# Kernel optimization log

Measured on AMD Instinct MI355X. Metric: run time of the kernel, lower is better.

## Reference

```python
import jax, jax.numpy as jnp
import numpy as np

N = 50000   # nodes
E = 800000  # edges
D = 128     # node feature dim
H = 128     # hidden channels
G = 500     # graphs
EPS = 1e-5


def setup_inputs() -> dict:
    key = jax.random.key(0)
    ks = jax.random.split(key, 12)
    s = 0.05
    inp = {
        'x': jax.random.normal(ks[0], (N, D), jnp.float32),
        'edge_index': jax.random.randint(ks[1], (2, E), 0, N, jnp.int64),
        'batch': jnp.sort(jax.random.randint(ks[2], (N,), 0, G, jnp.int64)),
        'W1': jax.random.normal(ks[3], (D, H), jnp.float32) * s,
        'b1': jnp.zeros((H,), jnp.float32),
        'g1': jnp.ones((H,), jnp.float32),
        'be1': jnp.zeros((H,), jnp.float32),
        'W2': jax.random.normal(ks[4], (H, H), jnp.float32) * s,
        'b2': jnp.zeros((H,), jnp.float32),
        'g2': jnp.ones((H,), jnp.float32),
        'be2': jnp.zeros((H,), jnp.float32),
        'W3': jax.random.normal(ks[5], (H, H), jnp.float32) * s,
        'b3': jnp.zeros((H,), jnp.float32),
        'g3': jnp.ones((H,), jnp.float32),
        'be3': jnp.zeros((H,), jnp.float32),
        'fcW1': jax.random.normal(ks[6], (H, H // 2), jnp.float32) * s,
        'fcb1': jnp.zeros((H // 2,), jnp.float32),
        'fcg1': jnp.ones((H // 2,), jnp.float32),
        'fcbe1': jnp.zeros((H // 2,), jnp.float32),
        'fcW2': jax.random.normal(ks[7], (H // 2, 1), jnp.float32) * s,
        'fcb2': jnp.zeros((1,), jnp.float32),
    }
    return inp


def _bn(h, g, b):
    # training-mode BatchNorm1d: batch stats, biased variance
    m = h.mean(0)
    v = jnp.mean((h - m) ** 2, 0)
    return g * (h - m) * jax.lax.rsqrt(v + EPS) + b


def reference(x, edge_index, batch, W1, b1, g1, be1, W2, b2, g2, be2,
              W3, b3, g3, be3, fcW1, fcb1, fcg1, fcbe1, fcW2, fcb2):
    # GCN normalization with self-loops: D^{-1/2}(A+I)D^{-1/2}
    loop = jnp.arange(N, dtype=edge_index.dtype)
    src = jnp.concatenate([edge_index[0], loop])
    dst = jnp.concatenate([edge_index[1], loop])
    deg = jax.ops.segment_sum(jnp.ones_like(dst, dtype=x.dtype), dst, N)
    dis = jax.lax.rsqrt(jnp.maximum(deg, 1.0))  # deg>=1 due to self loops
    norm = dis[src] * dis[dst]  # [E+N]

    def conv_bn_relu(h, W, b, g, be):
        h = h @ W                                   # [N,H]
        msg = h[src] * norm[:, None]                # gather + scale
        agg = jax.ops.segment_sum(msg, dst, N) + b  # scatter-add
        return jax.nn.relu(_bn(agg, g, be))

    h = conv_bn_relu(x, W1, b1, g1, be1)
    h = conv_bn_relu(h, W2, b2, g2, be2)
    h = conv_bn_relu(h, W3, b3, g3, be3)

    # global_mean_pool per graph
    cnt = jax.ops.segment_sum(jnp.ones((N,), h.dtype), batch, G)
    pooled = jax.ops.segment_sum(h, batch, G) / jnp.maximum(cnt, 1.0)[:, None]

    z = pooled @ fcW1 + fcb1
    z = jax.nn.relu(_bn(z, fcg1, fcbe1))
    return z @ fcW2 + fcb2  # [G,1]
```

## Files before the change

### kernel.cpp

```cpp
#include <hip/hip_runtime.h>

#define EPS 1e-5f
constexpr int HD = 128;
constexpr int FCD = 64;

typedef __attribute__((ext_vector_type(8))) short short8;
typedef __attribute__((ext_vector_type(4))) float floatx4;

__device__ inline ushort f2bf(float f){
  union{float f; unsigned u;} v; v.f = f;
  unsigned r = v.u + 0x7FFFu + ((v.u >> 16) & 1u);
  return (ushort)(r >> 16);
}
__device__ inline float bflo(unsigned u){ union{unsigned i; float f;} v; v.i = u << 16;        return v.f; }
__device__ inline float bfhi(unsigned u){ union{unsigned i; float f;} v; v.i = u & 0xFFFF0000u; return v.f; }
__device__ inline float bf2f(ushort u){ union{unsigned i; float f;} v; v.i = ((unsigned)u) << 16; return v.f; }


__global__ __launch_bounds__(256) void k_hist(const int* __restrict__ dst,
                                              int* __restrict__ bucketHist, int E){
  __shared__ int h[256];
  int t = threadIdx.x;
  h[t] = 0;
  __syncthreads();
  int base = blockIdx.x*4096;
  #pragma unroll
  for (int k = 0; k < 16; ++k){
    int e = base + k*256 + t;
    if (e < E) atomicAdd(&h[dst[e] >> 8], 1);
  }
  __syncthreads();
  if (h[t]) atomicAdd(&bucketHist[t], h[t]);
}

__global__ __launch_bounds__(256) void k_bscan(const int* __restrict__ bucketHist,
                                               int* __restrict__ bucketBase,
                                               int* __restrict__ bucketCursor){
  __shared__ int wt[4];
  int t = threadIdx.x, lane = t & 63, w = t >> 6;
  int v = bucketHist[t];
  int incl = v;
  #pragma unroll
  for (int o = 1; o < 64; o <<= 1){
    int x = __shfl_up(incl, o, 64);
    if (lane >= o) incl += x;
  }
  if (lane == 63) wt[w] = incl;
  __syncthreads();
  int woff = 0;
  for (int i = 0; i < w; ++i) woff += wt[i];
  int ex = woff + incl - v;
  bucketBase[t] = ex;
  bucketCursor[t] = ex;
}

__global__ __launch_bounds__(256) void k_bucket(const int* __restrict__ src,
                                                const int* __restrict__ dst,
                                                int* __restrict__ bucketCursor,
                                                int2* __restrict__ tmp, int E){
  __shared__ int h[256], ls[256], cur[256], gb[256];
  __shared__ int wt[4];
  __shared__ int2 staged[4096];
  __shared__ unsigned char bos[4096];
  int t = threadIdx.x, lane = t & 63, w = t >> 6;
  int base = blockIdx.x*4096;
  int2 ed[16]; int bk[16];
  h[t] = 0;
  __syncthreads();
  #pragma unroll
  for (int k = 0; k < 16; ++k){
    int e = base + k*256 + t;
    if (e < E){
      int s = src[e], d = dst[e];
      ed[k] = make_int2(s, d);
      bk[k] = d >> 8;
      atomicAdd(&h[bk[k]], 1);
    } else bk[k] = -1;
  }
  __syncthreads();
  int v = h[t];
  int incl = v;
  #pragma unroll
  for (int o = 1; o < 64; o <<= 1){
    int x = __shfl_up(incl, o, 64);
    if (lane >= o) incl += x;
  }
  if (lane == 63) wt[w] = incl;
  __syncthreads();
  int woff = 0;
  for (int i = 0; i < w; ++i) woff += wt[i];
  ls[t] = woff + incl - v;
  cur[t] = ls[t];
  if (v > 0) gb[t] = atomicAdd(&bucketCursor[t], v);
  __syncthreads();
  #pragma unroll
  for (int k = 0; k < 16; ++k){
    if (bk[k] >= 0){
      int lp = atomicAdd(&cur[bk[k]], 1);
      staged[lp] = ed[k];
      bos[lp] = (unsigned char)bk[k];
    }
  }
  __syncthreads();
  int nvalid = min(4096, E - base);
  #pragma unroll
  for (int k = 0; k < 16; ++k){
    int i = k*256 + t;
    if (i < nvalid){
      int b = bos[i];
      tmp[gb[b] + (i - ls[b])] = staged[i];
    }
  }
}

__global__ __launch_bounds__(256) void k_csr(const int2* __restrict__ tmp,
                                             const int* __restrict__ bucketHist,
                                             const int* __restrict__ bucketBase,
                                             int* __restrict__ rowptr,
                                             float* __restrict__ dis,
                                             int* __restrict__ csrc, int N){
  __shared__ int h[256], ls[256], cur[256];
  __shared__ int wt[4];
  __shared__ int stagedSrc[6144];
  int b = blockIdx.x, t = threadIdx.x, lane = t & 63, w = t >> 6;
  int ebase = bucketBase[b];
  int cnt = bucketHist[b];
  int node0 = b << 8;
  h[t] = 0;
  __syncthreads();
  for (int i = t; i < cnt; i += 256){
    int2 e = tmp[ebase + i];
    atomicAdd(&h[e.y - node0], 1);
  }
  __syncthreads();
  int v = h[t];
  int incl = v;
  #pragma unroll
  for (int o = 1; o < 64; o <<= 1){
    int x = __shfl_up(incl, o, 64);
    if (lane >= o) incl += x;
  }
  if (lane == 63) wt[w] = incl;
  __syncthreads();
  int woff = 0;
  for (int i = 0; i < w; ++i) woff += wt[i];
  int ex = woff + incl - v;
  ls[t] = ex; cur[t] = ex;
  int d = node0 + t;
  if (d < N){
    rowptr[d+1] = ebase + ex + v;
    dis[d] = rsqrtf((float)v + 1.0f);
  }
  if (b == 0 && t == 0) rowptr[0] = 0;
  __syncthreads();
  for (int i = t; i < cnt; i += 256){
    int2 e = tmp[ebase + i];
    int lp = atomicAdd(&cur[e.y - node0], 1);
    stagedSrc[lp] = e.x;
  }
  __syncthreads();
  for (int i = t; i < cnt; i += 256)
    csrc[ebase + i] = stagedSrc[i];
}

__global__ void k_prepW(const float* __restrict__ W1, const float* __restrict__ W2,
                        const float* __restrict__ W3, ushort* __restrict__ Wf){
  const float* Ws[3] = {W1, W2, W3};
  int l = blockIdx.y;
  int idx = blockIdx.x*256 + threadIdx.x;
  int k = idx >> 7, n = idx & 127;
  float w = Ws[l][idx];
  int kb = k >> 5, q = (k >> 3) & 3, j = k & 7;
  int nt = n >> 4, col = n & 15;
  Wf[(size_t)l*16384 + (((size_t)(kb*8 + nt)*64 + q*16 + col)*8 + j)] = f2bf(w);
}

template<int MODE>
__global__ __launch_bounds__(256) void k_gemm(const void* __restrict__ Av,
                                              const ushort* __restrict__ Wf,
                                              const float* __restrict__ sums,
                                              const float* __restrict__ g,
                                              const float* __restrict__ be,
                                              const float* __restrict__ dis,
                                              ushort* __restrict__ O, int n, float invN){
  __shared__ float aL[HD], bL[HD];
  int tid = threadIdx.x;
  if (MODE){
    if (tid < HD){
      float m = sums[tid]*invN;
      float var = fmaxf(sums[HD+tid]*invN - m*m, 0.f);
      float Ac = g[tid]*rsqrtf(var + EPS);
      aL[tid] = Ac; bL[tid] = be[tid] - m*Ac;
    }
    __syncthreads();
  }
  int lane = tid & 63, wave = tid >> 6;
  int quad = lane >> 4, r16 = lane & 15;
  int row = blockIdx.x*64 + wave*16 + r16;
  int rowc = min(row, n-1);
  floatx4 acc[8] = {};
  #pragma unroll
  for (int kb = 0; kb < 4; ++kb){
    int k0 = kb*32 + quad*8;
    short8 af;
    if (MODE){
      const ushort* Arow = (const ushort*)Av + (size_t)rowc*HD;
      short8 raw = *(const short8*)(Arow + k0);
      #pragma unroll
      for (int jj = 0; jj < 8; ++jj){
        float f = bf2f((ushort)raw[jj]);
        f = fmaxf(f*aL[k0+jj] + bL[k0+jj], 0.f);
        af[jj] = (short)f2bf(f);
      }
    } else {
      const float* Arow = (const float*)Av + (size_t)rowc*HD;
      float4 x0 = *(const float4*)(Arow + k0);
      float4 x1 = *(const float4*)(Arow + k0 + 4);
      af[0] = (short)f2bf(x0.x); af[1] = (short)f2bf(x0.y);
      af[2] = (short)f2bf(x0.z); af[3] = (short)f2bf(x0.w);
      af[4] = (short)f2bf(x1.x); af[5] = (short)f2bf(x1.y);
      af[6] = (short)f2bf(x1.z); af[7] = (short)f2bf(x1.w);
    }
    const ushort* wp = Wf + ((size_t)(kb*8)*64 + lane)*8;
    #pragma unroll
    for (int nt = 0; nt < 8; ++nt){
      short8 bf = *(const short8*)(wp + (size_t)nt*64*8);
      acc[nt] = __builtin_amdgcn_mfma_f32_16x16x32_bf16(af, bf, acc[nt], 0, 0, 0);
    }
  }
  int rbase = blockIdx.x*64 + wave*16 + quad*4;
  float ds[4];
  #pragma unroll
  for (int r = 0; r < 4; ++r) ds[r] = dis[min(rbase + r, n-1)];
  #pragma unroll
  for (int nt = 0; nt < 8; ++nt){
    #pragma unroll
    for (int r = 0; r < 4; ++r){
      int rr = rbase + r;
      if (rr < n) O[(size_t)rr*HD + nt*16 + r16] = f2bf(acc[nt][r]*ds[r]);
    }
  }
}

__global__ __launch_bounds__(256) void k_gather(const ushort* __restrict__ hw,
                                                const int* __restrict__ rowptr,
                                                const int* __restrict__ csrc,
                                                const float* __restrict__ dis,
                                                ushort* __restrict__ agg,
                                                float* __restrict__ scratch,
                                                float* __restrict__ sums, int N){
  __shared__ float2 sm[4][HD];
  if (blockIdx.x == 0) sums[threadIdx.x] = 0.f;
  int grp = threadIdx.x >> 4, j = threadIdx.x & 15;
  int wave = threadIdx.x >> 6, lane = threadIdx.x & 63;
  int i = blockIdx.x*16 + grp;
  bool valid = (i < N);
  int ic = valid ? i : N-1;
  uint4 q = ((const uint4*)(hw + (size_t)ic*HD))[j];
  float a[8];
  a[0] = bflo(q.x); a[1] = bfhi(q.x);
  a[2] = bflo(q.y); a[3] = bfhi(q.y);
  a[4] = bflo(q.z); a[5] = bfhi(q.z);
  a[6] = bflo(q.w); a[7] = bfhi(q.w);
  int e = rowptr[ic], e1 = rowptr[ic+1];
  #define ADD8(Q) \
    a[0] += bflo(Q.x); a[1] += bfhi(Q.x); \
    a[2] += bflo(Q.y); a[3] += bfhi(Q.y); \
    a[4] += bflo(Q.z); a[5] += bfhi(Q.z); \
    a[6] += bflo(Q.w); a[7] += bfhi(Q.w);
  while (e < e1 && (e & 3)){
    uint4 qq = ((const uint4*)(hw + (size_t)csrc[e]*HD))[j];
    ADD8(qq);
    e++;
  }
  int4 c0, c1;
  if (e + 8 <= e1){
    c0 = *(const int4*)&csrc[e];
    c1 = *(const int4*)&csrc[e+4];
  }
  while (e + 8 <= e1){
    int en = e + 8;
    int4 n0, n1;
    if (en + 8 <= e1){
      n0 = *(const int4*)&csrc[en];
      n1 = *(const int4*)&csrc[en+4];
    }
    uint4 q0 = ((const uint4*)(hw + (size_t)c0.x*HD))[j];
    uint4 q1 = ((const uint4*)(hw + (size_t)c0.y*HD))[j];
    uint4 q2 = ((const uint4*)(hw + (size_t)c0.z*HD))[j];
    uint4 q3 = ((const uint4*)(hw + (size_t)c0.w*HD))[j];
    uint4 q4 = ((const uint4*)(hw + (size_t)c1.x*HD))[j];
    uint4 q5 = ((const uint4*)(hw + (size_t)c1.y*HD))[j];
    uint4 q6 = ((const uint4*)(hw + (size_t)c1.z*HD))[j];
    uint4 q7 = ((const uint4*)(hw + (size_t)c1.w*HD))[j];
    ADD8(q0); ADD8(q1); ADD8(q2); ADD8(q3);
    ADD8(q4); ADD8(q5); ADD8(q6); ADD8(q7);
    c0 = n0; c1 = n1; e = en;
  }
  if (e + 4 <= e1){
    int4 tt = *(const int4*)&csrc[e];
    uint4 q0 = ((const uint4*)(hw + (size_t)tt.x*HD))[j];
    uint4 q1 = ((const uint4*)(hw + (size_t)tt.y*HD))[j];
    uint4 q2 = ((const uint4*)(hw + (size_t)tt.z*HD))[j];
    uint4 q3 = ((const uint4*)(hw + (size_t)tt.w*HD))[j];
    ADD8(q0); ADD8(q1); ADD8(q2); ADD8(q3);
    e += 4;
  }
  for (; e < e1; ++e){
    uint4 qq = ((const uint4*)(hw + (size_t)csrc[e]*HD))[j];
    ADD8(qq);
  }
  #undef ADD8
  float sc = dis[ic];
  #pragma unroll
  for (int k = 0; k < 8; ++k) a[k] *= sc;
  if (valid){
    uint4 o;
    o.x = (unsigned)f2bf(a[0]) | ((unsigned)f2bf(a[1]) << 16);
    o.y = (unsigned)f2bf(a[2]) | ((unsigned)f2bf(a[3]) << 16);
    o.z = (unsigned)f2bf(a[4]) | ((unsigned)f2bf(a[5]) << 16);
    o.w = (unsigned)f2bf(a[6]) | ((unsigned)f2bf(a[7]) << 16);
    ((uint4*)(agg + (size_t)i*HD))[j] = o;
  }
  float z = valid ? 1.f : 0.f;
  #pragma unroll
  for (int k = 0; k < 8; ++k){
    float s = a[k]*z, qq = a[k]*a[k]*z;
    s  += __shfl_xor(s, 16);  s  += __shfl_xor(s, 32);
    qq += __shfl_xor(qq, 16); qq += __shfl_xor(qq, 32);
    if (lane < 16) sm[wave][lane*8 + k] = make_float2(s, qq);
  }
  __syncthreads();
  int t = threadIdx.x;
  if (t < HD){
    float2 r0 = sm[0][t], r1 = sm[1][t], r2 = sm[2][t], r3 = sm[3][t];
    scratch[(size_t)blockIdx.x*256 + t]      = r0.x + r1.x + r2.x + r3.x;
    scratch[(size_t)blockIdx.x*256 + HD + t] = r0.y + r1.y + r2.y + r3.y;
  }
}

__global__ __launch_bounds__(256) void k_reduce(const float* __restrict__ scratch,
                                                float* __restrict__ sums, int R){
  int t = threadIdx.x;
  float acc = 0.f;
  for (int r = blockIdx.x; r < R; r += gridDim.x)
    acc += scratch[(size_t)r*256 + t];
  atomicAdd(&sums[t], acc);
}


__global__ __launch_bounds__(128) void k_pool(const ushort* __restrict__ h,
                                              const int* __restrict__ batch,
                                              const float* __restrict__ sums,
                                              const float* __restrict__ g,
                                              const float* __restrict__ be,
                                              float* __restrict__ pooled,
                                              float* __restrict__ cntf, int N, float invN){
  int c = threadIdx.x;
  float m = sums[c]*invN;
  float var = fmaxf(sums[HD+c]*invN - m*m, 0.f);
  float a = g[c]*rsqrtf(var + EPS);
  float b = be[c] - m*a;
  int start = blockIdx.x * 32;
  if (start >= N) return;
  int end = min(start + 32, N);
  int cur = batch[start];
  float acc = 0.f; int run = 0;
  for (int i = start; i < end; ++i){
    int bb = batch[i];
    if (bb != cur){
      atomicAdd(&pooled[(size_t)cur*HD + c], acc);
      if (c == 0) atomicAdd(&cntf[cur], (float)run);
      acc = 0.f; run = 0; cur = bb;
    }
    acc += fmaxf(bf2f(h[(size_t)i*HD + c])*a + b, 0.f);
    run++;
  }
  atomicAdd(&pooled[(size_t)cur*HD + c], acc);
  if (c == 0) atomicAdd(&cntf[cur], (float)run);
}


__global__ __launch_bounds__(64) void k_fc1(const float* __restrict__ pooled,
                                            const float* __restrict__ cntf,
                                            const float* __restrict__ W,
                                            const float* __restrict__ b,
                                            float* __restrict__ z,
                                            float* __restrict__ sums2, int G){
  int g = blockIdx.x, j = threadIdx.x;
  if (g == 0){ sums2[j] = 0.f; sums2[FCD + j] = 0.f; }
  float inv = 1.0f / fmaxf(cntf[g], 1.0f);
  float acc = 0.f;
  for (int k = 0; k < HD; ++k)
    acc += pooled[(size_t)g*HD + k] * W[k*FCD + j];
  z[(size_t)g*FCD + j] = acc * inv + b[j];
}

__global__ __launch_bounds__(64) void k_stats2(const float* __restrict__ z,
                                               float* __restrict__ sums2, int G){
  int c = threadIdx.x;
  float s = 0.f, q = 0.f;
  for (int i = blockIdx.x; i < G; i += gridDim.x){
    float v = z[(size_t)i*FCD + c]; s += v; q += v*v;
  }
  atomicAdd(&sums2[c], s);
  atomicAdd(&sums2[FCD + c], q);
}

__global__ __launch_bounds__(64) void k_final(const float* __restrict__ z,
                                              const float* __restrict__ sums2,
                                              const float* __restrict__ g,
                                              const float* __restrict__ be,
                                              const float* __restrict__ w2,
                                              const float* __restrict__ b2,
                                              float* __restrict__ out, int G, float invG){
  int gg = blockIdx.x, c = threadIdx.x;
  float m = sums2[c]*invG;
  float var = fmaxf(sums2[FCD+c]*invG - m*m, 0.f);
  float A = g[c]*rsqrtf(var + EPS);
  float B = be[c] - m*A;
  float v = fmaxf(z[(size_t)gg*FCD + c]*A + B, 0.f) * w2[c];
  #pragma unroll
  for (int o = 32; o > 0; o >>= 1) v += __shfl_down(v, o, 64);
  if (c == 0) out[gg] = v + b2[0];
}


extern "C" void kernel_launch(void* const* d_in, const int* in_sizes, int n_in,
                              void* d_out, int out_size, void* d_ws, size_t ws_size,
                              hipStream_t stream){
  const float* x    = (const float*)d_in[0];
  const int*   ei   = (const int*)d_in[1];
  const int*   batch= (const int*)d_in[2];
  const float* W1 = (const float*)d_in[3];
  const float* g1 = (const float*)d_in[5];
  const float* be1= (const float*)d_in[6];
  const float* W2 = (const float*)d_in[7];
  const float* g2 = (const float*)d_in[9];
  const float* be2= (const float*)d_in[10];
  const float* W3 = (const float*)d_in[11];
  const float* g3 = (const float*)d_in[13];
  const float* be3= (const float*)d_in[14];
  const float* fcW1 = (const float*)d_in[15];
  const float* fcb1 = (const float*)d_in[16];
  const float* fcg1 = (const float*)d_in[17];
  const float* fcbe1= (const float*)d_in[18];
  const float* fcW2 = (const float*)d_in[19];
  const float* fcb2 = (const float*)d_in[20];
  float* out = (float*)d_out;

  const int N = in_sizes[0] / HD;
  const int E = in_sizes[1] / 2;
  const int G = out_size;

  const int* esrc = ei;
  const int* edst = ei + E;

  char* p = (char*)d_ws;
  auto alloc = [&](size_t bytes)->void*{
    void* r = (void*)p; p += (bytes + 255) & ~(size_t)255; return r;
  };
  int gatherBlocks = (N + 15)/16;
  int nEB = (E + 4095)/4096;
  int NB  = (N + 255)/256;
  int*    bucketHist  = (int*) alloc(256*4);
  int*    bucketBase  = (int*) alloc(256*4);
  int*    bucketCursor= (int*) alloc(256*4);
  int2*   tmp    = (int2*)  alloc((size_t)E*8);
  int*    rowptr = (int*)   alloc((size_t)(N+1)*4);
  int*    csrc   = (int*)   alloc((size_t)E*4);
  float*  dis    = (float*) alloc((size_t)N*4);
  ushort* HWb    = (ushort*)alloc((size_t)N*HD*2);
  ushort* AGG    = (ushort*)alloc((size_t)N*HD*2);
  ushort* Wf     = (ushort*)alloc((size_t)3*HD*HD*2);
  float*  sums   = (float*) alloc(2*HD*4);
  float*  scratch= (float*) alloc((size_t)gatherBlocks*256*4);
  float*  pooled = (float*) alloc(((size_t)G*HD + G)*4);
  float*  cntf   = pooled + (size_t)G*HD;
  float*  zbuf   = (float*) alloc((size_t)G*FCD*4);
  float*  sums2  = (float*) alloc(2*FCD*4);

  float invN = 1.0f/(float)N, invG = 1.0f/(float)G;

  hipMemsetAsync(bucketHist, 0, 256*4, stream);
  k_hist  <<<nEB, 256, 0, stream>>>(edst, bucketHist, E);
  k_bscan <<<1, 256, 0, stream>>>(bucketHist, bucketBase, bucketCursor);
  k_bucket<<<nEB, 256, 0, stream>>>(esrc, edst, bucketCursor, tmp, E);
  k_csr   <<<NB, 256, 0, stream>>>(tmp, bucketHist, bucketBase, rowptr, dis, csrc, N);
  k_prepW <<<dim3(64,3), 256, 0, stream>>>(W1, W2, W3, Wf);

  int gemmBlocks = (N + 63)/64;

  k_gemm<0> <<<gemmBlocks, 256, 0, stream>>>(x,   Wf,         nullptr, nullptr, nullptr, dis, HWb, N, invN);
  k_gather  <<<gatherBlocks, 256, 0, stream>>>(HWb, rowptr, csrc, dis, AGG, scratch, sums, N);
  k_reduce  <<<64, 256, 0, stream>>>(scratch, sums, gatherBlocks);
  k_gemm<1> <<<gemmBlocks, 256, 0, stream>>>(AGG, Wf + 16384, sums, g1, be1, dis, HWb, N, invN);
  k_gather  <<<gatherBlocks, 256, 0, stream>>>(HWb, rowptr, csrc, dis, AGG, scratch, sums, N);
  k_reduce  <<<64, 256, 0, stream>>>(scratch, sums, gatherBlocks);
  k_gemm<1> <<<gemmBlocks, 256, 0, stream>>>(AGG, Wf + 32768, sums, g2, be2, dis, HWb, N, invN);
  k_gather  <<<gatherBlocks, 256, 0, stream>>>(HWb, rowptr, csrc, dis, AGG, scratch, sums, N);
  k_reduce  <<<64, 256, 0, stream>>>(scratch, sums, gatherBlocks);

  hipMemsetAsync(pooled, 0, ((size_t)G*HD + G)*4, stream);
  k_pool  <<<(N+31)/32, 128, 0, stream>>>(AGG, batch, sums, g3, be3, pooled, cntf, N, invN);
  k_fc1   <<<G, FCD, 0, stream>>>(pooled, cntf, fcW1, fcb1, zbuf, sums2, G);
  k_stats2<<<64, FCD, 0, stream>>>(zbuf, sums2, G);
  k_final <<<G, FCD, 0, stream>>>(zbuf, sums2, fcg1, fcbe1, fcW2, fcb2, out, G, invG);
}
```

Baseline: 359.2 us.

## Split node features into column panels and gather each panel in separate passes

Hidden features are now stored as four 32-column panels ([4][N][32] bf16) rather than row-major [N][128]. The gather runs once per panel, so each pass's random-access working set (about 3.2 MB) is more likely to stay cache-resident, at the cost of four times as many CSR index reads and more launches. The edge-bucketing temp is packed into one int per edge (16-bit src, 8-bit local dst), and the weight conversion and pooled-buffer zeroing are folded into the histogram kernel. The packing assumes N fits in 16 bits, which holds for these inputs but not in general.

```diff
diff --git a/kernel.cpp b/kernel.cpp
--- a/kernel.cpp
+++ b/kernel.cpp
@@ -16,21 +16,45 @@
 __device__ inline float bfhi(unsigned u){ union{unsigned i; float f;} v; v.i = u & 0xFFFF0000u; return v.f; }
 __device__ inline float bf2f(ushort u){ union{unsigned i; float f;} v; v.i = ((unsigned)u) << 16; return v.f; }
 
-
-__global__ __launch_bounds__(256) void k_hist(const int* __restrict__ dst,
-                                              int* __restrict__ bucketHist, int E){
+__global__ __launch_bounds__(256) void k_pre(const int* __restrict__ dst,
+                                             int* __restrict__ bucketHist, int E, int nEB,
+                                             const float* __restrict__ W1,
+                                             const float* __restrict__ W2,
+                                             const float* __restrict__ W3,
+                                             ushort* __restrict__ Wf,
+                                             float* __restrict__ pooled, int poolSz){
   __shared__ int h[256];
-  int t = threadIdx.x;
-  h[t] = 0;
-  __syncthreads();
-  int base = blockIdx.x*4096;
-  #pragma unroll
-  for (int k = 0; k < 16; ++k){
-    int e = base + k*256 + t;
-    if (e < E) atomicAdd(&h[dst[e] >> 8], 1);
-  }
-  __syncthreads();
-  if (h[t]) atomicAdd(&bucketHist[t], h[t]);
+  int bid = blockIdx.x, t = threadIdx.x;
+  if (bid < nEB){
+    h[t] = 0;
+    __syncthreads();
+    int base = bid*4096;
+    #pragma unroll
+    for (int k = 0; k < 16; ++k){
+      int e = base + k*256 + t;
+      if (e < E) atomicAdd(&h[dst[e] >> 8], 1);
+    }
+    __syncthreads();
+    if (h[t]) atomicAdd(&bucketHist[t], h[t]);
+  } else if (bid < nEB + 192){
+    int j = bid - nEB;
+    int l = j >> 6;
+    int idx = (j & 63)*256 + t;
+    const float* W = (l == 0) ? W1 : (l == 1) ? W2 : W3;
+    float w = W[idx];
+    int k = idx >> 7, n = idx & 127;
+    int kb = k >> 5, q4 = (k >> 3) & 3, jj = k & 7;
+    int nt = n >> 4, col = n & 15;
+    Wf[(size_t)l*16384 + (((size_t)(kb*8 + nt)*64 + q4*16 + col)*8 + jj)] = f2bf(w);
+  } else {
+    int j = bid - nEB - 192;
+    int base = (j*256 + t)*4;
+    #pragma unroll
+    for (int k = 0; k < 4; ++k){
+      int o = base + k;
+      if (o < poolSz) pooled[o] = 0.f;
+    }
+  }
 }
 
 __global__ __launch_bounds__(256) void k_bscan(const int* __restrict__ bucketHist,
@@ -57,14 +81,14 @@
 __global__ __launch_bounds__(256) void k_bucket(const int* __restrict__ src,
                                                 const int* __restrict__ dst,
                                                 int* __restrict__ bucketCursor,
-                                                int2* __restrict__ tmp, int E){
+                                                int* __restrict__ tmp, int E){
   __shared__ int h[256], ls[256], cur[256], gb[256];
   __shared__ int wt[4];
-  __shared__ int2 staged[4096];
+  __shared__ int staged[4096];
   __shared__ unsigned char bos[4096];
   int t = threadIdx.x, lane = t & 63, w = t >> 6;
   int base = blockIdx.x*4096;
-  int2 ed[16]; int bk[16];
+  int ed[16]; int bk[16];
   h[t] = 0;
   __syncthreads();
   #pragma unroll
@@ -72,7 +96,7 @@
     int e = base + k*256 + t;
     if (e < E){
       int s = src[e], d = dst[e];
-      ed[k] = make_int2(s, d);
+      ed[k] = s | ((d & 255) << 16);
       bk[k] = d >> 8;
       atomicAdd(&h[bk[k]], 1);
     } else bk[k] = -1;
@@ -113,7 +137,7 @@
   }
 }
 
-__global__ __launch_bounds__(256) void k_csr(const int2* __restrict__ tmp,
+__global__ __launch_bounds__(256) void k_csr(const int* __restrict__ tmp,
                                              const int* __restrict__ bucketHist,
                                              const int* __restrict__ bucketBase,
                                              int* __restrict__ rowptr,
@@ -128,10 +152,8 @@
   int node0 = b << 8;
   h[t] = 0;
   __syncthreads();
-  for (int i = t; i < cnt; i += 256){
-    int2 e = tmp[ebase + i];
-    atomicAdd(&h[e.y - node0], 1);
-  }
+  for (int i = t; i < cnt; i += 256)
+    atomicAdd(&h[(tmp[ebase + i] >> 16) & 255], 1);
   __syncthreads();
   int v = h[t];
   int incl = v;
@@ -154,25 +176,13 @@
   if (b == 0 && t == 0) rowptr[0] = 0;
   __syncthreads();
   for (int i = t; i < cnt; i += 256){
-    int2 e = tmp[ebase + i];
-    int lp = atomicAdd(&cur[e.y - node0], 1);
-    stagedSrc[lp] = e.x;
+    int e = tmp[ebase + i];
+    int lp = atomicAdd(&cur[(e >> 16) & 255], 1);
+    stagedSrc[lp] = e & 0xFFFF;
   }
   __syncthreads();
   for (int i = t; i < cnt; i += 256)
     csrc[ebase + i] = stagedSrc[i];
-}
-
-__global__ void k_prepW(const float* __restrict__ W1, const float* __restrict__ W2,
-                        const float* __restrict__ W3, ushort* __restrict__ Wf){
-  const float* Ws[3] = {W1, W2, W3};
-  int l = blockIdx.y;
-  int idx = blockIdx.x*256 + threadIdx.x;
-  int k = idx >> 7, n = idx & 127;
-  float w = Ws[l][idx];
-  int kb = k >> 5, q = (k >> 3) & 3, j = k & 7;
-  int nt = n >> 4, col = n & 15;
-  Wf[(size_t)l*16384 + (((size_t)(kb*8 + nt)*64 + q*16 + col)*8 + j)] = f2bf(w);
 }
 
 template<int MODE>
@@ -204,8 +214,8 @@
     int k0 = kb*32 + quad*8;
     short8 af;
     if (MODE){
-      const ushort* Arow = (const ushort*)Av + (size_t)rowc*HD;
-      short8 raw = *(const short8*)(Arow + k0);
+      const ushort* Ap = (const ushort*)Av + ((size_t)kb*n + rowc)*32 + quad*8;
+      short8 raw = *(const short8*)Ap;
       #pragma unroll
       for (int jj = 0; jj < 8; ++jj){
         float f = bf2f((ushort)raw[jj]);
@@ -234,29 +244,34 @@
   for (int r = 0; r < 4; ++r) ds[r] = dis[min(rbase + r, n-1)];
   #pragma unroll
   for (int nt = 0; nt < 8; ++nt){
+    int p = nt >> 1, cp = (nt & 1)*16 + r16;
     #pragma unroll
     for (int r = 0; r < 4; ++r){
       int rr = rbase + r;
-      if (rr < n) O[(size_t)rr*HD + nt*16 + r16] = f2bf(acc[nt][r]*ds[r]);
-    }
-  }
-}
-
-__global__ __launch_bounds__(256) void k_gather(const ushort* __restrict__ hw,
-                                                const int* __restrict__ rowptr,
-                                                const int* __restrict__ csrc,
-                                                const float* __restrict__ dis,
-                                                ushort* __restrict__ agg,
-                                                float* __restrict__ scratch,
-                                                float* __restrict__ sums, int N){
-  __shared__ float2 sm[4][HD];
-  if (blockIdx.x == 0) sums[threadIdx.x] = 0.f;
-  int grp = threadIdx.x >> 4, j = threadIdx.x & 15;
-  int wave = threadIdx.x >> 6, lane = threadIdx.x & 63;
-  int i = blockIdx.x*16 + grp;
+      if (rr < n) O[((size_t)p*n + rr)*32 + cp] = f2bf(acc[nt][r]*ds[r]);
+    }
+  }
+}
+
+__global__ __launch_bounds__(256) void k_gatherp(const ushort* __restrict__ hwAll,
+                                                 const int* __restrict__ rowptr,
+                                                 const int* __restrict__ csrc,
+                                                 const float* __restrict__ dis,
+                                                 ushort* __restrict__ aggAll,
+                                                 float* __restrict__ scratch,
+                                                 float* __restrict__ sums,
+                                                 int N, int pass, int NBg){
+  __shared__ float2 sm[4][32];
+  if (pass == 0 && blockIdx.x == 0) sums[threadIdx.x] = 0.f;
+  const ushort* hw = hwAll + (size_t)pass*N*32;
+  ushort* agg = aggAll + (size_t)pass*N*32;
+  int t = threadIdx.x;
+  int nodein = t >> 2, cg = t & 3;
+  int wave = t >> 6, lane = t & 63;
+  int i = blockIdx.x*64 + nodein;
   bool valid = (i < N);
   int ic = valid ? i : N-1;
-  uint4 q = ((const uint4*)(hw + (size_t)ic*HD))[j];
+  uint4 q = *(const uint4*)(hw + (size_t)ic*32 + cg*8);
   float a[8];
   a[0] = bflo(q.x); a[1] = bfhi(q.x);
   a[2] = bflo(q.y); a[3] = bfhi(q.y);
@@ -269,7 +284,7 @@
     a[4] += bflo(Q.z); a[5] += bfhi(Q.z); \
     a[6] += bflo(Q.w); a[7] += bfhi(Q.w);
   while (e < e1 && (e & 3)){
-    uint4 qq = ((const uint4*)(hw + (size_t)csrc[e]*HD))[j];
+    uint4 qq = *(const uint4*)(hw + (size_t)csrc[e]*32 + cg*8);
     ADD8(qq);
     e++;
   }
@@ -285,29 +300,29 @@
       n0 = *(const int4*)&csrc[en];
       n1 = *(const int4*)&csrc[en+4];
     }
-    uint4 q0 = ((const uint4*)(hw + (size_t)c0.x*HD))[j];
-    uint4 q1 = ((const uint4*)(hw + (size_t)c0.y*HD))[j];
-    uint4 q2 = ((const uint4*)(hw + (size_t)c0.z*HD))[j];
-    uint4 q3 = ((const uint4*)(hw + (size_t)c0.w*HD))[j];
-    uint4 q4 = ((const uint4*)(hw + (size_t)c1.x*HD))[j];
-    uint4 q5 = ((const uint4*)(hw + (size_t)c1.y*HD))[j];
-    uint4 q6 = ((const uint4*)(hw + (size_t)c1.z*HD))[j];
-    uint4 q7 = ((const uint4*)(hw + (size_t)c1.w*HD))[j];
+    uint4 q0 = *(const uint4*)(hw + (size_t)c0.x*32 + cg*8);
+    uint4 q1 = *(const uint4*)(hw + (size_t)c0.y*32 + cg*8);
+    uint4 q2 = *(const uint4*)(hw + (size_t)c0.z*32 + cg*8);
+    uint4 q3 = *(const uint4*)(hw + (size_t)c0.w*32 + cg*8);
+    uint4 q4 = *(const uint4*)(hw + (size_t)c1.x*32 + cg*8);
+    uint4 q5 = *(const uint4*)(hw + (size_t)c1.y*32 + cg*8);
+    uint4 q6 = *(const uint4*)(hw + (size_t)c1.z*32 + cg*8);
+    uint4 q7 = *(const uint4*)(hw + (size_t)c1.w*32 + cg*8);
     ADD8(q0); ADD8(q1); ADD8(q2); ADD8(q3);
     ADD8(q4); ADD8(q5); ADD8(q6); ADD8(q7);
     c0 = n0; c1 = n1; e = en;
   }
   if (e + 4 <= e1){
     int4 tt = *(const int4*)&csrc[e];
-    uint4 q0 = ((const uint4*)(hw + (size_t)tt.x*HD))[j];
-    uint4 q1 = ((const uint4*)(hw + (size_t)tt.y*HD))[j];
-    uint4 q2 = ((const uint4*)(hw + (size_t)tt.z*HD))[j];
-    uint4 q3 = ((const uint4*)(hw + (size_t)tt.w*HD))[j];
+    uint4 q0 = *(const uint4*)(hw + (size_t)tt.x*32 + cg*8);
+    uint4 q1 = *(const uint4*)(hw + (size_t)tt.y*32 + cg*8);
+    uint4 q2 = *(const uint4*)(hw + (size_t)tt.z*32 + cg*8);
+    uint4 q3 = *(const uint4*)(hw + (size_t)tt.w*32 + cg*8);
     ADD8(q0); ADD8(q1); ADD8(q2); ADD8(q3);
     e += 4;
   }
   for (; e < e1; ++e){
-    uint4 qq = ((const uint4*)(hw + (size_t)csrc[e]*HD))[j];
+    uint4 qq = *(const uint4*)(hw + (size_t)csrc[e]*32 + cg*8);
     ADD8(qq);
   }
   #undef ADD8
@@ -320,34 +335,42 @@
     o.y = (unsigned)f2bf(a[2]) | ((unsigned)f2bf(a[3]) << 16);
     o.z = (unsigned)f2bf(a[4]) | ((unsigned)f2bf(a[5]) << 16);
     o.w = (unsigned)f2bf(a[6]) | ((unsigned)f2bf(a[7]) << 16);
-    ((uint4*)(agg + (size_t)i*HD))[j] = o;
+    *(uint4*)(agg + (size_t)i*32 + cg*8) = o;
   }
   float z = valid ? 1.f : 0.f;
+  float rs[8], rq[8];
   #pragma unroll
   for (int k = 0; k < 8; ++k){
     float s = a[k]*z, qq = a[k]*a[k]*z;
-    s  += __shfl_xor(s, 16);  s  += __shfl_xor(s, 32);
-    qq += __shfl_xor(qq, 16); qq += __shfl_xor(qq, 32);
-    if (lane < 16) sm[wave][lane*8 + k] = make_float2(s, qq);
-  }
-  __syncthreads();
+    s  += __shfl_xor(s, 4);  s  += __shfl_xor(s, 8);  s  += __shfl_xor(s, 16);  s  += __shfl_xor(s, 32);
+    qq += __shfl_xor(qq, 4); qq += __shfl_xor(qq, 8); qq += __shfl_xor(qq, 16); qq += __shfl_xor(qq, 32);
+    rs[k] = s; rq[k] = qq;
+  }
+  if (lane < 4){
+    #pragma unroll
+    for (int k = 0; k < 8; ++k) sm[wave][lane*8 + k] = make_float2(rs[k], rq[k]);
+  }
+  __syncthreads();
+  size_t base = ((size_t)pass*NBg + blockIdx.x)*64;
+  if (t < 32)
+    scratch[base + t] = sm[0][t].x + sm[1][t].x + sm[2][t].x + sm[3][t].x;
+  else if (t < 64){
+    int c = t - 32;
+    scratch[base + t] = sm[0][c].y + sm[1][c].y + sm[2][c].y + sm[3][c].y;
+  }
+}
+
+__global__ __launch_bounds__(256) void k_reduce(const float* __restrict__ scratch,
+                                                float* __restrict__ sums, int NBg){
   int t = threadIdx.x;
-  if (t < HD){
-    float2 r0 = sm[0][t], r1 = sm[1][t], r2 = sm[2][t], r3 = sm[3][t];
-    scratch[(size_t)blockIdx.x*256 + t]      = r0.x + r1.x + r2.x + r3.x;
-    scratch[(size_t)blockIdx.x*256 + HD + t] = r0.y + r1.y + r2.y + r3.y;
-  }
-}
-
-__global__ __launch_bounds__(256) void k_reduce(const float* __restrict__ scratch,
-                                                float* __restrict__ sums, int R){
-  int t = threadIdx.x;
+  int isq = t >> 7;
+  int c = t & 127;
+  int p = c >> 5, cc = c & 31;
   float acc = 0.f;
-  for (int r = blockIdx.x; r < R; r += gridDim.x)
-    acc += scratch[(size_t)r*256 + t];
+  for (int b = blockIdx.x; b < NBg; b += gridDim.x)
+    acc += scratch[((size_t)p*NBg + b)*64 + isq*32 + cc];
   atomicAdd(&sums[t], acc);
 }
-
 
 __global__ __launch_bounds__(128) void k_pool(const ushort* __restrict__ h,
                                               const int* __restrict__ batch,
@@ -361,6 +384,7 @@
   float var = fmaxf(sums[HD+c]*invN - m*m, 0.f);
   float a = g[c]*rsqrtf(var + EPS);
   float b = be[c] - m*a;
+  const ushort* hp = h + (size_t)(c >> 5)*N*32 + (c & 31);
   int start = blockIdx.x * 32;
   if (start >= N) return;
   int end = min(start + 32, N);
@@ -373,7 +397,7 @@
       if (c == 0) atomicAdd(&cntf[cur], (float)run);
       acc = 0.f; run = 0; cur = bb;
     }
-    acc += fmaxf(bf2f(h[(size_t)i*HD + c])*a + b, 0.f);
+    acc += fmaxf(bf2f(hp[(size_t)i*32])*a + b, 0.f);
     run++;
   }
   atomicAdd(&pooled[(size_t)cur*HD + c], acc);
@@ -460,13 +484,15 @@
   auto alloc = [&](size_t bytes)->void*{
     void* r = (void*)p; p += (bytes + 255) & ~(size_t)255; return r;
   };
-  int gatherBlocks = (N + 15)/16;
+  int NBg = (N + 63)/64;
   int nEB = (E + 4095)/4096;
   int NB  = (N + 255)/256;
+  int poolSz = G*HD + G;
+  int PZ = (poolSz + 1023)/1024;
   int*    bucketHist  = (int*) alloc(256*4);
   int*    bucketBase  = (int*) alloc(256*4);
   int*    bucketCursor= (int*) alloc(256*4);
-  int2*   tmp    = (int2*)  alloc((size_t)E*8);
+  int*    tmp    = (int*)   alloc((size_t)E*4);
   int*    rowptr = (int*)   alloc((size_t)(N+1)*4);
   int*    csrc   = (int*)   alloc((size_t)E*4);
   float*  dis    = (float*) alloc((size_t)N*4);
@@ -474,7 +500,7 @@
   ushort* AGG    = (ushort*)alloc((size_t)N*HD*2);
   ushort* Wf     = (ushort*)alloc((size_t)3*HD*HD*2);
   float*  sums   = (float*) alloc(2*HD*4);
-  float*  scratch= (float*) alloc((size_t)gatherBlocks*256*4);
+  float*  scratch= (float*) alloc((size_t)4*NBg*64*4);
   float*  pooled = (float*) alloc(((size_t)G*HD + G)*4);
   float*  cntf   = pooled + (size_t)G*HD;
   float*  zbuf   = (float*) alloc((size_t)G*FCD*4);
@@ -483,25 +509,27 @@
   float invN = 1.0f/(float)N, invG = 1.0f/(float)G;
 
   hipMemsetAsync(bucketHist, 0, 256*4, stream);
-  k_hist  <<<nEB, 256, 0, stream>>>(edst, bucketHist, E);
+  k_pre   <<<nEB + 192 + PZ, 256, 0, stream>>>(edst, bucketHist, E, nEB,
+                                               W1, W2, W3, Wf, pooled, poolSz);
   k_bscan <<<1, 256, 0, stream>>>(bucketHist, bucketBase, bucketCursor);
   k_bucket<<<nEB, 256, 0, stream>>>(esrc, edst, bucketCursor, tmp, E);
   k_csr   <<<NB, 256, 0, stream>>>(tmp, bucketHist, bucketBase, rowptr, dis, csrc, N);
-  k_prepW <<<dim3(64,3), 256, 0, stream>>>(W1, W2, W3, Wf);
 
   int gemmBlocks = (N + 63)/64;
 
   k_gemm<0> <<<gemmBlocks, 256, 0, stream>>>(x,   Wf,         nullptr, nullptr, nullptr, dis, HWb, N, invN);
-  k_gather  <<<gatherBlocks, 256, 0, stream>>>(HWb, rowptr, csrc, dis, AGG, scratch, sums, N);
-  k_reduce  <<<64, 256, 0, stream>>>(scratch, sums, gatherBlocks);
+  for (int pp = 0; pp < 4; ++pp)
+    k_gatherp<<<NBg, 256, 0, stream>>>(HWb, rowptr, csrc, dis, AGG, scratch, sums, N, pp, NBg);
+  k_reduce  <<<64, 256, 0, stream>>>(scratch, sums, NBg);
   k_gemm<1> <<<gemmBlocks, 256, 0, stream>>>(AGG, Wf + 16384, sums, g1, be1, dis, HWb, N, invN);
-  k_gather  <<<gatherBlocks, 256, 0, stream>>>(HWb, rowptr, csrc, dis, AGG, scratch, sums, N);
-  k_reduce  <<<64, 256, 0, stream>>>(scratch, sums, gatherBlocks);
+  for (int pp = 0; pp < 4; ++pp)
+    k_gatherp<<<NBg, 256, 0, stream>>>(HWb, rowptr, csrc, dis, AGG, scratch, sums, N, pp, NBg);
+  k_reduce  <<<64, 256, 0, stream>>>(scratch, sums, NBg);
   k_gemm<1> <<<gemmBlocks, 256, 0, stream>>>(AGG, Wf + 32768, sums, g2, be2, dis, HWb, N, invN);
-  k_gather  <<<gatherBlocks, 256, 0, stream>>>(HWb, rowptr, csrc, dis, AGG, scratch, sums, N);
-  k_reduce  <<<64, 256, 0, stream>>>(scratch, sums, gatherBlocks);
-
-  hipMemsetAsync(pooled, 0, ((size_t)G*HD + G)*4, stream);
+  for (int pp = 0; pp < 4; ++pp)
+    k_gatherp<<<NBg, 256, 0, stream>>>(HWb, rowptr, csrc, dis, AGG, scratch, sums, N, pp, NBg);
+  k_reduce  <<<64, 256, 0, stream>>>(scratch, sums, NBg);
+
   k_pool  <<<(N+31)/32, 128, 0, stream>>>(AGG, batch, sums, g3, be3, pooled, cntf, N, invN);
   k_fc1   <<<G, FCD, 0, stream>>>(pooled, cntf, fcW1, fcb1, zbuf, sums2, G);
   k_stats2<<<64, FCD, 0, stream>>>(zbuf, sums2, G);
```

Result: slower. 377.1 us (+5.0%).

## Merge setup kernels, pack edge pairs into one int, fold FC stats

Applied to the files above, without the earlier changes.

Merges the histogram, weight-repack and pooled-buffer zeroing into one launch, which replaces a separate kernel and a memset. The bucketed edge temp array shrinks from int2 to a single int packing src (16 bits) with the low 8 bits of dst, halving that traffic. The FC batch-norm statistics are accumulated with atomics inside k_fc1, so k_stats2 is gone, and sums2 is now zeroed in k_pool. The packing assumes src < 65536, which holds for N=50000 but would break on larger graphs.

```diff
diff --git a/kernel.cpp b/kernel.cpp
--- a/kernel.cpp
+++ b/kernel.cpp
@@ -16,21 +16,45 @@
 __device__ inline float bfhi(unsigned u){ union{unsigned i; float f;} v; v.i = u & 0xFFFF0000u; return v.f; }
 __device__ inline float bf2f(ushort u){ union{unsigned i; float f;} v; v.i = ((unsigned)u) << 16; return v.f; }
 
-
-__global__ __launch_bounds__(256) void k_hist(const int* __restrict__ dst,
-                                              int* __restrict__ bucketHist, int E){
+__global__ __launch_bounds__(256) void k_pre(const int* __restrict__ dst,
+                                             int* __restrict__ bucketHist, int E, int nEB,
+                                             const float* __restrict__ W1,
+                                             const float* __restrict__ W2,
+                                             const float* __restrict__ W3,
+                                             ushort* __restrict__ Wf,
+                                             float* __restrict__ pooled, int poolSz){
   __shared__ int h[256];
-  int t = threadIdx.x;
-  h[t] = 0;
-  __syncthreads();
-  int base = blockIdx.x*4096;
-  #pragma unroll
-  for (int k = 0; k < 16; ++k){
-    int e = base + k*256 + t;
-    if (e < E) atomicAdd(&h[dst[e] >> 8], 1);
-  }
-  __syncthreads();
-  if (h[t]) atomicAdd(&bucketHist[t], h[t]);
+  int bid = blockIdx.x, t = threadIdx.x;
+  if (bid < nEB){
+    h[t] = 0;
+    __syncthreads();
+    int base = bid*4096;
+    #pragma unroll
+    for (int k = 0; k < 16; ++k){
+      int e = base + k*256 + t;
+      if (e < E) atomicAdd(&h[dst[e] >> 8], 1);
+    }
+    __syncthreads();
+    if (h[t]) atomicAdd(&bucketHist[t], h[t]);
+  } else if (bid < nEB + 192){
+    int j = bid - nEB;
+    int l = j >> 6;
+    int idx = (j & 63)*256 + t;
+    const float* W = (l == 0) ? W1 : (l == 1) ? W2 : W3;
+    float w = W[idx];
+    int k = idx >> 7, n = idx & 127;
+    int kb = k >> 5, q4 = (k >> 3) & 3, jj = k & 7;
+    int nt = n >> 4, col = n & 15;
+    Wf[(size_t)l*16384 + (((size_t)(kb*8 + nt)*64 + q4*16 + col)*8 + jj)] = f2bf(w);
+  } else {
+    int j = bid - nEB - 192;
+    int base = (j*256 + t)*4;
+    #pragma unroll
+    for (int k = 0; k < 4; ++k){
+      int o = base + k;
+      if (o < poolSz) pooled[o] = 0.f;
+    }
+  }
 }
 
 __global__ __launch_bounds__(256) void k_bscan(const int* __restrict__ bucketHist,
@@ -57,14 +81,14 @@
 __global__ __launch_bounds__(256) void k_bucket(const int* __restrict__ src,
                                                 const int* __restrict__ dst,
                                                 int* __restrict__ bucketCursor,
-                                                int2* __restrict__ tmp, int E){
+                                                int* __restrict__ tmp, int E){
   __shared__ int h[256], ls[256], cur[256], gb[256];
   __shared__ int wt[4];
-  __shared__ int2 staged[4096];
+  __shared__ int staged[4096];
   __shared__ unsigned char bos[4096];
   int t = threadIdx.x, lane = t & 63, w = t >> 6;
   int base = blockIdx.x*4096;
-  int2 ed[16]; int bk[16];
+  int ed[16]; int bk[16];
   h[t] = 0;
   __syncthreads();
   #pragma unroll
@@ -72,7 +96,7 @@
     int e = base + k*256 + t;
     if (e < E){
       int s = src[e], d = dst[e];
-      ed[k] = make_int2(s, d);
+      ed[k] = s | ((d & 255) << 16);
       bk[k] = d >> 8;
       atomicAdd(&h[bk[k]], 1);
     } else bk[k] = -1;
@@ -113,7 +137,7 @@
   }
 }
 
-__global__ __launch_bounds__(256) void k_csr(const int2* __restrict__ tmp,
+__global__ __launch_bounds__(256) void k_csr(const int* __restrict__ tmp,
                                              const int* __restrict__ bucketHist,
                                              const int* __restrict__ bucketBase,
                                              int* __restrict__ rowptr,
@@ -128,10 +152,8 @@
   int node0 = b << 8;
   h[t] = 0;
   __syncthreads();
-  for (int i = t; i < cnt; i += 256){
-    int2 e = tmp[ebase + i];
-    atomicAdd(&h[e.y - node0], 1);
-  }
+  for (int i = t; i < cnt; i += 256)
+    atomicAdd(&h[(tmp[ebase + i] >> 16) & 255], 1);
   __syncthreads();
   int v = h[t];
   int incl = v;
@@ -154,25 +176,13 @@
   if (b == 0 && t == 0) rowptr[0] = 0;
   __syncthreads();
   for (int i = t; i < cnt; i += 256){
-    int2 e = tmp[ebase + i];
-    int lp = atomicAdd(&cur[e.y - node0], 1);
-    stagedSrc[lp] = e.x;
+    int e = tmp[ebase + i];
+    int lp = atomicAdd(&cur[(e >> 16) & 255], 1);
+    stagedSrc[lp] = e & 0xFFFF;
   }
   __syncthreads();
   for (int i = t; i < cnt; i += 256)
     csrc[ebase + i] = stagedSrc[i];
-}
-
-__global__ void k_prepW(const float* __restrict__ W1, const float* __restrict__ W2,
-                        const float* __restrict__ W3, ushort* __restrict__ Wf){
-  const float* Ws[3] = {W1, W2, W3};
-  int l = blockIdx.y;
-  int idx = blockIdx.x*256 + threadIdx.x;
-  int k = idx >> 7, n = idx & 127;
-  float w = Ws[l][idx];
-  int kb = k >> 5, q = (k >> 3) & 3, j = k & 7;
-  int nt = n >> 4, col = n & 15;
-  Wf[(size_t)l*16384 + (((size_t)(kb*8 + nt)*64 + q*16 + col)*8 + j)] = f2bf(w);
 }
 
 template<int MODE>
@@ -348,15 +358,16 @@
   atomicAdd(&sums[t], acc);
 }
 
-
 __global__ __launch_bounds__(128) void k_pool(const ushort* __restrict__ h,
                                               const int* __restrict__ batch,
                                               const float* __restrict__ sums,
                                               const float* __restrict__ g,
                                               const float* __restrict__ be,
                                               float* __restrict__ pooled,
-                                              float* __restrict__ cntf, int N, float invN){
+                                              float* __restrict__ cntf,
+                                              float* __restrict__ sums2, int N, float invN){
   int c = threadIdx.x;
+  if (blockIdx.x == 0) sums2[c] = 0.f;
   float m = sums[c]*invN;
   float var = fmaxf(sums[HD+c]*invN - m*m, 0.f);
   float a = g[c]*rsqrtf(var + EPS);
@@ -388,23 +399,14 @@
                                             float* __restrict__ z,
                                             float* __restrict__ sums2, int G){
   int g = blockIdx.x, j = threadIdx.x;
-  if (g == 0){ sums2[j] = 0.f; sums2[FCD + j] = 0.f; }
   float inv = 1.0f / fmaxf(cntf[g], 1.0f);
   float acc = 0.f;
   for (int k = 0; k < HD; ++k)
     acc += pooled[(size_t)g*HD + k] * W[k*FCD + j];
-  z[(size_t)g*FCD + j] = acc * inv + b[j];
-}
-
-__global__ __launch_bounds__(64) void k_stats2(const float* __restrict__ z,
-                                               float* __restrict__ sums2, int G){
-  int c = threadIdx.x;
-  float s = 0.f, q = 0.f;
-  for (int i = blockIdx.x; i < G; i += gridDim.x){
-    float v = z[(size_t)i*FCD + c]; s += v; q += v*v;
-  }
-  atomicAdd(&sums2[c], s);
-  atomicAdd(&sums2[FCD + c], q);
+  float zv = acc * inv + b[j];
+  z[(size_t)g*FCD + j] = zv;
+  atomicAdd(&sums2[j], zv);
+  atomicAdd(&sums2[FCD + j], zv*zv);
 }
 
 __global__ __launch_bounds__(64) void k_final(const float* __restrict__ z,
@@ -463,10 +465,12 @@
   int gatherBlocks = (N + 15)/16;
   int nEB = (E + 4095)/4096;
   int NB  = (N + 255)/256;
+  int poolSz = G*HD + G;
+  int PZ = (poolSz + 1023)/1024;
   int*    bucketHist  = (int*) alloc(256*4);
   int*    bucketBase  = (int*) alloc(256*4);
   int*    bucketCursor= (int*) alloc(256*4);
-  int2*   tmp    = (int2*)  alloc((size_t)E*8);
+  int*    tmp    = (int*)   alloc((size_t)E*4);
   int*    rowptr = (int*)   alloc((size_t)(N+1)*4);
   int*    csrc   = (int*)   alloc((size_t)E*4);
   float*  dis    = (float*) alloc((size_t)N*4);
@@ -483,11 +487,11 @@
   float invN = 1.0f/(float)N, invG = 1.0f/(float)G;
 
   hipMemsetAsync(bucketHist, 0, 256*4, stream);
-  k_hist  <<<nEB, 256, 0, stream>>>(edst, bucketHist, E);
+  k_pre   <<<nEB + 192 + PZ, 256, 0, stream>>>(edst, bucketHist, E, nEB,
+                                               W1, W2, W3, Wf, pooled, poolSz);
   k_bscan <<<1, 256, 0, stream>>>(bucketHist, bucketBase, bucketCursor);
   k_bucket<<<nEB, 256, 0, stream>>>(esrc, edst, bucketCursor, tmp, E);
   k_csr   <<<NB, 256, 0, stream>>>(tmp, bucketHist, bucketBase, rowptr, dis, csrc, N);
-  k_prepW <<<dim3(64,3), 256, 0, stream>>>(W1, W2, W3, Wf);
 
   int gemmBlocks = (N + 63)/64;
 
@@ -501,9 +505,7 @@
   k_gather  <<<gatherBlocks, 256, 0, stream>>>(HWb, rowptr, csrc, dis, AGG, scratch, sums, N);
   k_reduce  <<<64, 256, 0, stream>>>(scratch, sums, gatherBlocks);
 
-  hipMemsetAsync(pooled, 0, ((size_t)G*HD + G)*4, stream);
-  k_pool  <<<(N+31)/32, 128, 0, stream>>>(AGG, batch, sums, g3, be3, pooled, cntf, N, invN);
+  k_pool  <<<(N+31)/32, 128, 0, stream>>>(AGG, batch, sums, g3, be3, pooled, cntf, sums2, N, invN);
   k_fc1   <<<G, FCD, 0, stream>>>(pooled, cntf, fcW1, fcb1, zbuf, sums2, G);
-  k_stats2<<<64, FCD, 0, stream>>>(zbuf, sums2, G);
   k_final <<<G, FCD, 0, stream>>>(zbuf, sums2, fcg1, fcbe1, fcW2, fcb2, out, G, invG);
 }
```

Result: no change. 366.3 us (+2.0%).
